# Performance work log

Hardware: AMD Instinct MI355X
Metric: run time of the kernel (lower is better)

## Reference

```python
import jax, jax.numpy as jnp
import numpy as np

B, S, H = 2, 2048, 2048
NH, NKV, HD = 8, 2, 256
WIN = 512
EPS = 1e-6
WAV = 10000.0


def _rms_norm(x, scale=None, eps=EPS):
    # Gemma3n RMSNorm: normalize in float32 over last dim, optional learned scale.
    x32 = x.astype(jnp.float32)
    n = x32 * jax.lax.rsqrt(jnp.mean(x32 * x32, axis=-1, keepdims=True) + eps)
    if scale is not None:
        n = n * scale
    return n.astype(x.dtype)


def _rope(x):
    # keras-hub RotaryEmbedding (half-split rotation). x: [B, S, nheads, hd]
    s, hd = x.shape[1], x.shape[-1]
    inv_freq = 1.0 / (WAV ** (jnp.arange(0, hd, 2, dtype=jnp.float32) / hd))  # [hd/2]
    freqs = jnp.arange(s, dtype=jnp.float32)[:, None] * inv_freq[None, :]      # [S, hd/2]
    cos = jnp.cos(freqs)[None, :, None, :]
    sin = jnp.sin(freqs)[None, :, None, :]
    x1, x2 = jnp.split(x, 2, axis=-1)
    return jnp.concatenate([x1 * cos - x2 * sin, x2 * cos + x1 * sin], axis=-1)


def setup_inputs() -> dict:
    key = jax.random.key(0)
    ks = jax.random.split(key, 8)
    hidden_states = jax.random.normal(ks[0], (B, S, H), dtype=jnp.float32)
    # causal mask [B, S, S]
    causal = jnp.tril(jnp.ones((S, S), dtype=bool))
    attention_mask = jnp.broadcast_to(causal[None], (B, S, S))
    sd = 1.0 / np.sqrt(H)
    Wq = jax.random.normal(ks[1], (H, NH * HD), dtype=jnp.float32) * sd
    Wk = jax.random.normal(ks[2], (H, NKV * HD), dtype=jnp.float32) * sd
    Wv = jax.random.normal(ks[3], (H, NKV * HD), dtype=jnp.float32) * sd
    Wo = jax.random.normal(ks[4], (NH * HD, H), dtype=jnp.float32) * (1.0 / np.sqrt(NH * HD))
    q_scale = jnp.ones((HD,), jnp.float32) + 0.02 * jax.random.normal(ks[5], (HD,), dtype=jnp.float32)
    k_scale = jnp.ones((HD,), jnp.float32) + 0.02 * jax.random.normal(ks[6], (HD,), dtype=jnp.float32)
    return {"hidden_states": hidden_states, "attention_mask": attention_mask,
            "Wq": Wq, "Wk": Wk, "Wv": Wv, "Wo": Wo,
            "q_scale": q_scale, "k_scale": k_scale}


def reference(hidden_states, attention_mask, Wq, Wk, Wv, Wo, q_scale, k_scale):
    b, s, _ = hidden_states.shape
    # Q: proj -> per-head RMSNorm -> RoPE -> [B, NH, S, HD]
    q = (hidden_states @ Wq).reshape(b, s, NH, HD)
    q = jnp.transpose(_rope(_rms_norm(q, q_scale)), (0, 2, 1, 3))
    # K: proj -> RMSNorm -> RoPE; V: proj -> RMSNorm (no scale, no RoPE)
    k = (hidden_states @ Wk).reshape(b, s, NKV, HD)
    k = jnp.transpose(_rope(_rms_norm(k, k_scale)), (0, 2, 1, 3))
    v = jnp.transpose(_rms_norm((hidden_states @ Wv).reshape(b, s, NKV, HD)), (0, 2, 1, 3))
    # GQA repeat_kv (groups = NH // NKV)
    g = NH // NKV
    k = jnp.repeat(k, g, axis=1)
    v = jnp.repeat(v, g, axis=1)
    # scores with scaling = 1.0 (as in source)
    scores = jnp.einsum('bhqd,bhkd->bhqk', q, k)
    # sliding-window band AND user causal mask
    idx = jnp.arange(s)
    band = jnp.abs(idx[:, None] - idx[None, :]) <= (WIN - 1)  # [S, S]
    mask = attention_mask.astype(bool) & band[None]           # [B, S, S]
    scores = jnp.where(mask[:, None], scores, -1e9)
    attn = jax.nn.softmax(scores, axis=-1)
    out = jnp.einsum('bhqk,bhkd->bhqd', attn, v)
    out = jnp.transpose(out, (0, 2, 1, 3)).reshape(b, s, NH * HD)
    return out @ Wo
```

## Files before the change

kernel.cpp:

```cpp
#include <hip/hip_runtime.h>
#include <cstdint>
#include <cstddef>

typedef unsigned short u16;
typedef float floatx4 __attribute__((ext_vector_type(4)));
typedef __bf16 bf16x8 __attribute__((ext_vector_type(8)));

__device__ __forceinline__ u16 f2bf(float f) {
  union { float f; unsigned u; } v;
  v.f = f;
  unsigned u = v.u;
  u += 0x7FFFu + ((u >> 16) & 1u);
  return (u16)(u >> 16);
}
__device__ __forceinline__ float bf2f(u16 h) {
  union { unsigned u; float f; } v;
  v.u = ((unsigned)h) << 16;
  return v.f;
}

#define GLL16(g, l)                                                       \
  __builtin_amdgcn_global_load_lds(                                       \
      (const __attribute__((address_space(1))) void*)(g),                 \
      (__attribute__((address_space(3))) void*)(l), 16, 0, 0)

__global__ __launch_bounds__(256) void prep_all(
    const float* __restrict__ X, u16* __restrict__ Xh, u16* __restrict__ Xl,
    const float* __restrict__ Wq, const float* __restrict__ Wk,
    const float* __restrict__ Wv, const float* __restrict__ Wo,
    u16* __restrict__ Wth, u16* __restrict__ Wot, float* __restrict__ ct,
    float* __restrict__ st) {
  __shared__ u16 T[64][80];
  const int blk = blockIdx.x, t = threadIdx.x;
  if (blk < 4096) {
    const int idx = blk * 256 + t;
    float x[8];
    *(float4*)&x[0] = *(const float4*)(X + (size_t)idx * 8);
    *(float4*)&x[4] = *(const float4*)(X + (size_t)idx * 8 + 4);
    u16 h[8], l[8];
#pragma unroll
    for (int j = 0; j < 8; ++j) {
      h[j] = f2bf(x[j]);
      l[j] = f2bf(x[j] - bf2f(h[j]));
    }
    *(uint4*)(Xh + (size_t)idx * 8) = *(const uint4*)h;
    *(uint4*)(Xl + (size_t)idx * 8) = *(const uint4*)l;
    return;
  }
  if (blk >= 6656) {
    const int idx = (blk - 6656) * 256 + t;
    const int s = idx >> 7, fi = idx & 127;
    const float invf = expf((float)fi * (-9.210340371976184f / 128.f));
    float sv, cv;
    sincosf((float)s * invf, &sv, &cv);
    ct[idx] = cv;
    st[idx] = sv;
    return;
  }
  const float* in;
  u16* out;
  int C, tt, gx, gy;
  if (blk < 5120) {
    in = Wq; out = Wth; C = 2048; tt = blk - 4096; gx = tt & 31; gy = tt >> 5;
  } else if (blk < 5376) {
    in = Wk; out = Wth + (size_t)2048 * 2048; C = 512; tt = blk - 5120;
    gx = tt & 7; gy = tt >> 3;
  } else if (blk < 5632) {
    in = Wv; out = Wth + (size_t)2560 * 2048; C = 512; tt = blk - 5376;
    gx = tt & 7; gy = tt >> 3;
  } else {
    in = Wo; out = Wot; C = 2048; tt = blk - 5632; gx = tt & 31; gy = tt >> 5;
  }
  const int r0 = gy * 64, c0 = gx * 64;
#pragma unroll
  for (int p = 0; p < 4; ++p) {
    const int rl = (t >> 4) + p * 16;
    const int c4 = (t & 15) * 4;
    float4 v = *(const float4*)(in + (size_t)(r0 + rl) * C + c0 + c4);
    T[c4 + 0][rl] = f2bf(v.x);
    T[c4 + 1][rl] = f2bf(v.y);
    T[c4 + 2][rl] = f2bf(v.z);
    T[c4 + 3][rl] = f2bf(v.w);
  }
  __syncthreads();
#pragma unroll
  for (int p = 0; p < 2; ++p) {
    const int cl = (t >> 3) + p * 32;
    const int r8 = (t & 7) * 8;
    *(uint4*)(out + (size_t)(c0 + cl) * 2048 + r0 + r8) =
        *(const uint4*)&T[cl][r8];
  }
}

__global__ __launch_bounds__(256) void gemm_qkv2(
    const u16* __restrict__ Ah, const u16* __restrict__ Al,
    const u16* __restrict__ Bt_all, float* __restrict__ Cq,
    float* __restrict__ Ckv, int K) {
  __shared__ u16 Ash[2][4096], Asl[2][4096], Bs[2][4096];
  const int tid = threadIdx.x;
  const int lane = tid & 63;
  const int wid = tid >> 6;
  const int g = lane >> 4, lc = lane & 15;
  const int gsw = g ^ ((lc >> 1) & 3);
  const int lbs = lc * 32 + gsw * 8;
  const int lin = blockIdx.x;
  const u16* Bt;
  float* C;
  int N, nwg, gridx, lin_s;
  if (lin < 512) {
    Bt = Bt_all; C = Cq; N = 2048; nwg = 512; gridx = 16; lin_s = lin;
  } else {
    Bt = Bt_all + (size_t)2048 * 2048; C = Ckv; N = 1024; nwg = 256;
    gridx = 8; lin_s = lin - 512;
  }
  const int swz = (lin_s & 7) * (nwg >> 3) + (lin_s >> 3);
  const int bm = (swz / gridx) * 128, bn = (swz % gridx) * 128;
  const int wr = (wid >> 1) * 64, wc = (wid & 1) * 64;
  const int xk8 = (((tid & 3) ^ ((tid >> 3) & 3)) * 8);
  const size_t aoff = (size_t)(bm + (tid >> 2)) * K + xk8;
  const size_t boff = (size_t)(bn + (tid >> 2)) * K + xk8;

  floatx4 acc[4][4];
#pragma unroll
  for (int i = 0; i < 4; ++i)
#pragma unroll
    for (int j = 0; j < 4; ++j) acc[i][j] = floatx4{0.f, 0.f, 0.f, 0.f};

  GLL16(Ah + aoff, Ash[0] + tid * 8);
  GLL16(Ah + aoff + (size_t)64 * K, Ash[0] + 2048 + tid * 8);
  GLL16(Al + aoff, Asl[0] + tid * 8);
  GLL16(Al + aoff + (size_t)64 * K, Asl[0] + 2048 + tid * 8);
  GLL16(Bt + boff, Bs[0] + tid * 8);
  GLL16(Bt + boff + (size_t)64 * K, Bs[0] + 2048 + tid * 8);
  int cur = 0;

  for (int k0 = 0; k0 < K; k0 += 32) {
    __syncthreads();
    if (k0 + 32 < K) {
      const int kn = k0 + 32;
      GLL16(Ah + aoff + kn, Ash[cur ^ 1] + tid * 8);
      GLL16(Ah + aoff + (size_t)64 * K + kn, Ash[cur ^ 1] + 2048 + tid * 8);
      GLL16(Al + aoff + kn, Asl[cur ^ 1] + tid * 8);
      GLL16(Al + aoff + (size_t)64 * K + kn, Asl[cur ^ 1] + 2048 + tid * 8);
      GLL16(Bt + boff + kn, Bs[cur ^ 1] + tid * 8);
      GLL16(Bt + boff + (size_t)64 * K + kn, Bs[cur ^ 1] + 2048 + tid * 8);
    }
    bf16x8 afh[4], afl[4], bfr[4];
#pragma unroll
    for (int m = 0; m < 4; ++m) {
      afh[m] = *(const bf16x8*)(Ash[cur] + (wr + m * 16) * 32 + lbs);
      afl[m] = *(const bf16x8*)(Asl[cur] + (wr + m * 16) * 32 + lbs);
    }
#pragma unroll
    for (int n = 0; n < 4; ++n)
      bfr[n] = *(const bf16x8*)(Bs[cur] + (wc + n * 16) * 32 + lbs);
#pragma unroll
    for (int m = 0; m < 4; ++m)
#pragma unroll
      for (int n = 0; n < 4; ++n) {
        acc[m][n] = __builtin_amdgcn_mfma_f32_16x16x32_bf16(afh[m], bfr[n],
                                                            acc[m][n], 0, 0, 0);
        acc[m][n] = __builtin_amdgcn_mfma_f32_16x16x32_bf16(afl[m], bfr[n],
                                                            acc[m][n], 0, 0, 0);
      }
    cur ^= 1;
  }
#pragma unroll
  for (int m = 0; m < 4; ++m)
#pragma unroll
    for (int n = 0; n < 4; ++n) {
      float* Cp = C + (size_t)(bm + wr + m * 16 + g * 4) * N + bn + wc +
                  n * 16 + lc;
#pragma unroll
      for (int r = 0; r < 4; ++r) Cp[(size_t)r * N] = acc[m][n][r];
    }
}

__global__ __launch_bounds__(256) void gemm_bf16(const u16* __restrict__ A,
                                                 const u16* __restrict__ Bt,
                                                 float* __restrict__ C, int M,
                                                 int N, int K) {
  __shared__ u16 As[2][4096];
  __shared__ u16 Bs[2][4096];
  const int tid = threadIdx.x;
  const int lane = tid & 63;
  const int wid = tid >> 6;
  const int g = lane >> 4, lc = lane & 15;
  const int gsw = g ^ ((lc >> 1) & 3);
  const int lbs = lc * 32 + gsw * 8;
  const int nwg = gridDim.x * gridDim.y;
  const int lin = blockIdx.y * gridDim.x + blockIdx.x;
  const int swz = (lin & 7) * (nwg >> 3) + (lin >> 3);
  const int bm = (swz / gridDim.x) * 128, bn = (swz % gridDim.x) * 128;
  const int wr = (wid >> 1) * 64, wc = (wid & 1) * 64;
  const int xk8 = (((tid & 3) ^ ((tid >> 3) & 3)) * 8);
  const u16* Ag = A + (size_t)(bm + (tid >> 2)) * K + xk8;
  const u16* Bg = Bt + (size_t)(bn + (tid >> 2)) * K + xk8;

  floatx4 acc[4][4];
#pragma unroll
  for (int i = 0; i < 4; ++i)
#pragma unroll
    for (int j = 0; j < 4; ++j) acc[i][j] = floatx4{0.f, 0.f, 0.f, 0.f};

  GLL16(Ag, As[0] + tid * 8);
  GLL16(Ag + (size_t)64 * K, As[0] + 2048 + tid * 8);
  GLL16(Bg, Bs[0] + tid * 8);
  GLL16(Bg + (size_t)64 * K, Bs[0] + 2048 + tid * 8);
  int cur = 0;

  for (int k0 = 0; k0 < K; k0 += 32) {
    __syncthreads();
    if (k0 + 32 < K) {
      const int kn = k0 + 32;
      GLL16(Ag + kn, As[cur ^ 1] + tid * 8);
      GLL16(Ag + (size_t)64 * K + kn, As[cur ^ 1] + 2048 + tid * 8);
      GLL16(Bg + kn, Bs[cur ^ 1] + tid * 8);
      GLL16(Bg + (size_t)64 * K + kn, Bs[cur ^ 1] + 2048 + tid * 8);
    }
    bf16x8 af[4], bfr[4];
#pragma unroll
    for (int m = 0; m < 4; ++m)
      af[m] = *(const bf16x8*)(As[cur] + (wr + m * 16) * 32 + lbs);
#pragma unroll
    for (int n = 0; n < 4; ++n)
      bfr[n] = *(const bf16x8*)(Bs[cur] + (wc + n * 16) * 32 + lbs);
#pragma unroll
    for (int m = 0; m < 4; ++m)
#pragma unroll
      for (int n = 0; n < 4; ++n)
        acc[m][n] = __builtin_amdgcn_mfma_f32_16x16x32_bf16(af[m], bfr[n],
                                                            acc[m][n], 0, 0, 0);
    cur ^= 1;
  }
#pragma unroll
  for (int m = 0; m < 4; ++m)
#pragma unroll
    for (int n = 0; n < 4; ++n) {
      float* Cp = C + (size_t)(bm + wr + m * 16 + g * 4) * N + bn + wc +
                  n * 16 + lc;
#pragma unroll
      for (int r = 0; r < 4; ++r) Cp[(size_t)r * N] = acc[m][n][r];
    }
}

__global__ __launch_bounds__(256) void rmsrope2(
    const float* __restrict__ qproj, const float* __restrict__ kvproj,
    u16* __restrict__ qph, u16* __restrict__ qpl, u16* __restrict__ kph,
    u16* __restrict__ kpl, u16* __restrict__ vpk,
    const float* __restrict__ q_scale, const float* __restrict__ k_scale,
    const float* __restrict__ ct, const float* __restrict__ st) {
  __shared__ u16 nh[32][264], nl[32][264];
  const int t = threadIdx.x, lane = t & 63, w = t >> 6;
  const int blk = blockIdx.x;
  const int slot = blk % 12;
  const int rt = blk / 12;
  const int bs0 = rt * 32;
  const int b = bs0 >> 11;
  const int s0 = bs0 & 2047;
  const float* srcb;
  const float* scale = nullptr;
  int srccol, srcstride;
  bool rope;
  if (slot < 8) {
    srcb = qproj; srccol = slot * 256; srcstride = 2048; scale = q_scale;
    rope = true;
  } else if (slot < 10) {
    srcb = kvproj; srccol = (slot - 8) * 256; srcstride = 1024;
    scale = k_scale; rope = true;
  } else {
    srcb = kvproj; srccol = 512 + (slot - 10) * 256; srcstride = 1024;
    rope = false;
  }
  const int d0 = lane * 4;
  float4 sc4 = make_float4(1.f, 1.f, 1.f, 1.f);
  if (scale) sc4 = *(const float4*)(scale + d0);
  const int fi4 = (lane & 31) * 4;

#pragma unroll
  for (int rr = 0; rr < 8; ++rr) {
    const int r = w * 8 + rr;
    const int s = s0 + r;
    float4 x = *(const float4*)(srcb + (size_t)(bs0 + r) * srcstride + srccol +
                                d0);
    float ss = x.x * x.x + x.y * x.y + x.z * x.z + x.w * x.w;
#pragma unroll
    for (int off = 32; off; off >>= 1) ss += __shfl_xor(ss, off);
    const float inv = rsqrtf(ss * (1.f / 256.f) + 1e-6f);
    float4 n;
    n.x = x.x * inv * sc4.x;
    n.y = x.y * inv * sc4.y;
    n.z = x.z * inv * sc4.z;
    n.w = x.w * inv * sc4.w;
    if (rope) {
      float4 p;
      p.x = __shfl_xor(n.x, 32);
      p.y = __shfl_xor(n.y, 32);
      p.z = __shfl_xor(n.z, 32);
      p.w = __shfl_xor(n.w, 32);
      const float4 cv = *(const float4*)(ct + s * 128 + fi4);
      const float4 sv = *(const float4*)(st + s * 128 + fi4);
      if (lane < 32) {
        n.x = n.x * cv.x - p.x * sv.x;
        n.y = n.y * cv.y - p.y * sv.y;
        n.z = n.z * cv.z - p.z * sv.z;
        n.w = n.w * cv.w - p.w * sv.w;
      } else {
        n.x = n.x * cv.x + p.x * sv.x;
        n.y = n.y * cv.y + p.y * sv.y;
        n.z = n.z * cv.z + p.z * sv.z;
        n.w = n.w * cv.w + p.w * sv.w;
      }
    }
    const float nv[4] = {n.x, n.y, n.z, n.w};
#pragma unroll
    for (int j = 0; j < 4; ++j) {
      const u16 hh = f2bf(nv[j]);
      nh[r][d0 + j] = hh;
      nl[r][d0 + j] = f2bf(nv[j] - bf2f(hh));
    }
  }
  __syncthreads();

  if (slot < 8) {
    u16* dh = qph + (((size_t)(b * 8 + slot) * 128 + (s0 >> 4)) * 4096);
    u16* dl = qpl + (((size_t)(b * 8 + slot) * 128 + (s0 >> 4)) * 4096);
#pragma unroll
    for (int p = 0; p < 4; ++p) {
      const int gi = p * 256 + t;
      const int tile = gi >> 9, kc = (gi >> 6) & 7, lc2 = (gi >> 2) & 15,
                gg = gi & 3;
      const int row = tile * 16 + lc2, col = kc * 32 + gg * 8;
      *(uint4*)(dh + (size_t)gi * 8) = *(const uint4*)&nh[row][col];
      *(uint4*)(dl + (size_t)gi * 8) = *(const uint4*)&nl[row][col];
    }
  } else if (slot < 10) {
    const int kvh = slot - 8;
    u16* dh = kph + (((size_t)(b * 2 + kvh) * 64 + (s0 >> 5)) * 8192);
    u16* dl = kpl + (((size_t)(b * 2 + kvh) * 64 + (s0 >> 5)) * 8192);
#pragma unroll
    for (int p = 0; p < 4; ++p) {
      const int gi = p * 256 + t;
      const int kc = gi >> 7, hi = (gi >> 6) & 1, lc2 = (gi >> 2) & 15,
                gg = gi & 3;
      const int ggs = gg ^ ((lc2 >> 1) & 3);
      const int row = hi * 16 + lc2, col = kc * 32 + gg * 8;
      const size_t off = kc * 1024 + hi * 512 + lc2 * 32 + ggs * 8;
      *(uint4*)(dh + off) = *(const uint4*)&nh[row][col];
      *(uint4*)(dl + off) = *(const uint4*)&nl[row][col];
    }
  } else {
    const int kvh = slot - 10;
    u16* dv = vpk + (((size_t)(b * 2 + kvh) * 64 + (s0 >> 5)) * 8192);
#pragma unroll
    for (int p = 0; p < 4; ++p) {
      const int gi = p * 256 + t;
      const int di = gi >> 6, lc2 = (gi >> 2) & 15, gg = gi & 3;
      const int ggs = gg ^ ((lc2 >> 1) & 3);
      u16 tmp[8];
#pragma unroll
      for (int e = 0; e < 8; ++e) tmp[e] = nh[gg * 8 + e][di * 16 + lc2];
      *(uint4*)(dv + (size_t)(di * 512 + lc2 * 32 + ggs * 8)) =
          *(const uint4*)tmp;
    }
  }
}

__global__ __launch_bounds__(512) void attn_mfma5(
    const u16* __restrict__ qph, const u16* __restrict__ qpl,
    const u16* __restrict__ kph, const u16* __restrict__ kpl,
    const u16* __restrict__ vpk, u16* __restrict__ attnb) {
  __shared__ u16 SH[54272];
  u16* const KhB = SH;
  u16* const KlB = SH + 16384;
  u16* const VB = SH + 32768;
  const int tid = threadIdx.x, lane = tid & 63, wid = tid >> 6;
  const int g = lane >> 4, lc = lane & 15;
  const int lbu = lc * 32 + g * 8;
  const int lbs = lc * 32 + (g ^ ((lc >> 1) & 3)) * 8;
  const int lin = blockIdx.x;
  const int swz = (lin & 7) * 32 + (lin >> 3);
  const int qt = swz & 15;
  const int h = (swz >> 4) & 7;
  const int b = swz >> 7;
  const int kvh = h >> 2;
  const int i0b = qt * 128;
  const int i0 = i0b + wid * 16;

  bf16x8 qfh[8], qfl[8];
  {
    const size_t qtb = ((size_t)(b * 8 + h) * 128 + (i0 >> 4)) * 4096 + lbu;
#pragma unroll
    for (int kc = 0; kc < 8; ++kc) {
      qfh[kc] = *(const bf16x8*)(qph + qtb + kc * 512);
      qfl[kc] = *(const bf16x8*)(qpl + qtb + kc * 512);
    }
  }
  floatx4 o[16];
#pragma unroll
  for (int d = 0; d < 16; ++d) o[d] = floatx4{0.f, 0.f, 0.f, 0.f};
  float m_[4] = {-1e20f, -1e20f, -1e20f, -1e20f};
  float l_[4] = {0.f, 0.f, 0.f, 0.f};
  u16* pw = SH + 49152 + wid * 640;

  const int jlo = (i0b >= 512) ? i0b - 512 : 0;
  const int nt = (i0b + 128 - jlo) >> 5;
  const size_t kvbase = (size_t)(b * 2 + kvh) * 64;
  const int t0 = jlo >> 5;

  {
    const size_t tb = (kvbase + t0) * 8192;
    GLL16(kph + tb + tid * 8, KhB + tid * 8);
    GLL16(kph + tb + 4096 + tid * 8, KhB + 4096 + tid * 8);
    GLL16(kpl + tb + tid * 8, KlB + tid * 8);
    GLL16(kpl + tb + 4096 + tid * 8, KlB + 4096 + tid * 8);
    GLL16(vpk + tb + tid * 8, VB + tid * 8);
    GLL16(vpk + tb + 4096 + tid * 8, VB + 4096 + tid * 8);
  }
  int cur = 0;

  for (int t = 0; t < nt; ++t) {
    __syncthreads();
    if (t + 1 < nt) {
      const size_t tb = (kvbase + t0 + t + 1) * 8192;
      const int nb = (cur ^ 1) * 8192;
      GLL16(kph + tb + tid * 8, KhB + nb + tid * 8);
      GLL16(kph + tb + 4096 + tid * 8, KhB + nb + 4096 + tid * 8);
      GLL16(kpl + tb + tid * 8, KlB + nb + tid * 8);
      GLL16(kpl + tb + 4096 + tid * 8, KlB + nb + 4096 + tid * 8);
      GLL16(vpk + tb + tid * 8, VB + nb + tid * 8);
      GLL16(vpk + tb + 4096 + tid * 8, VB + nb + 4096 + tid * 8);
    }
    const int j0 = jlo + t * 32;
    if (!(j0 > i0 + 15 || j0 + 31 < i0 - 511)) {
      const u16* Kh = KhB + cur * 8192;
      const u16* Kl = KlB + cur * 8192;
      floatx4 s0h = floatx4{0.f, 0.f, 0.f, 0.f}, s0x = s0h, s0y = s0h;
      floatx4 s1h = s0h, s1x = s0h, s1y = s0h;
      __builtin_amdgcn_s_setprio(1);
#pragma unroll
      for (int kc = 0; kc < 8; ++kc) {
        const bf16x8 kh0 = *(const bf16x8*)(Kh + kc * 1024 + lbs);
        const bf16x8 kh1 = *(const bf16x8*)(Kh + kc * 1024 + 512 + lbs);
        const bf16x8 kl0 = *(const bf16x8*)(Kl + kc * 1024 + lbs);
        const bf16x8 kl1 = *(const bf16x8*)(Kl + kc * 1024 + 512 + lbs);
        s0h = __builtin_amdgcn_mfma_f32_16x16x32_bf16(qfh[kc], kh0, s0h, 0, 0, 0);
        s1h = __builtin_amdgcn_mfma_f32_16x16x32_bf16(qfh[kc], kh1, s1h, 0, 0, 0);
        s0x = __builtin_amdgcn_mfma_f32_16x16x32_bf16(qfh[kc], kl0, s0x, 0, 0, 0);
        s1x = __builtin_amdgcn_mfma_f32_16x16x32_bf16(qfh[kc], kl1, s1x, 0, 0, 0);
        s0y = __builtin_amdgcn_mfma_f32_16x16x32_bf16(qfl[kc], kh0, s0y, 0, 0, 0);
        s1y = __builtin_amdgcn_mfma_f32_16x16x32_bf16(qfl[kc], kh1, s1y, 0, 0, 0);
      }
      __builtin_amdgcn_s_setprio(0);
      floatx4 s0 = s0h + s0x + s0y;
      floatx4 s1 = s1h + s1x + s1y;
      if (!(j0 + 31 <= i0 && (i0 + 15) - j0 <= 511)) {
        const int ja = j0 + lc, jb_ = j0 + 16 + lc;
#pragma unroll
        for (int r = 0; r < 4; ++r) {
          const int i = i0 + g * 4 + r;
          if (ja > i || i - ja > 511) s0[r] = -1e30f;
          if (jb_ > i || i - jb_ > 511) s1[r] = -1e30f;
        }
      }
      float rmax[4], p0[4], p1[4], sc[4], rs[4];
#pragma unroll
      for (int r = 0; r < 4; ++r) rmax[r] = fmaxf(s0[r], s1[r]);
#pragma unroll
      for (int off = 1; off < 16; off <<= 1)
#pragma unroll
        for (int r = 0; r < 4; ++r)
          rmax[r] = fmaxf(rmax[r], __shfl_xor(rmax[r], off));
#pragma unroll
      for (int r = 0; r < 4; ++r) {
        const float mn = fmaxf(m_[r], rmax[r]);
        sc[r] = __expf(m_[r] - mn);
        m_[r] = mn;
        p0[r] = __expf(s0[r] - mn);
        p1[r] = __expf(s1[r] - mn);
        rs[r] = p0[r] + p1[r];
      }
#pragma unroll
      for (int off = 1; off < 16; off <<= 1)
#pragma unroll
        for (int r = 0; r < 4; ++r) rs[r] += __shfl_xor(rs[r], off);
#pragma unroll
      for (int r = 0; r < 4; ++r) l_[r] = l_[r] * sc[r] + rs[r];
#pragma unroll
      for (int r = 0; r < 4; ++r) {
        pw[(g * 4 + r) * 40 + lc] = f2bf(p0[r]);
        pw[(g * 4 + r) * 40 + 16 + lc] = f2bf(p1[r]);
      }
#pragma unroll
      for (int d = 0; d < 16; ++d)
#pragma unroll
        for (int r = 0; r < 4; ++r) o[d][r] *= sc[r];
      const bf16x8 pf = *(const bf16x8*)(pw + lc * 40 + g * 8);
      const u16* Vt = VB + cur * 8192;
      __builtin_amdgcn_s_setprio(1);
#pragma unroll
      for (int d = 0; d < 16; ++d)
        o[d] = __builtin_amdgcn_mfma_f32_16x16x32_bf16(
            pf, *(const bf16x8*)(Vt + d * 512 + lbs), o[d], 0, 0, 0);
      __builtin_amdgcn_s_setprio(0);
    }
    cur ^= 1;
  }
  float rinv[4];
#pragma unroll
  for (int r = 0; r < 4; ++r) rinv[r] = 1.f / l_[r];
  __syncthreads();
  u16* ow = SH + wid * 4224;
#pragma unroll
  for (int d = 0; d < 16; ++d)
#pragma unroll
    for (int r = 0; r < 4; ++r)
      ow[(g * 4 + r) * 264 + d * 16 + lc] = f2bf(o[d][r] * rinv[r]);
  u16* orow = attnb + ((size_t)(b * 2048 + i0) * 2048 + h * 256);
#pragma unroll
  for (int p = 0; p < 8; ++p) {
    const int gi = p * 64 + lane;
    const int row = gi >> 5, ch = gi & 31;
    *(uint4*)(orow + (size_t)row * 2048 + ch * 8) =
        *(const uint4*)(ow + row * 264 + ch * 8);
  }
}

extern "C" void kernel_launch(void* const* d_in, const int* in_sizes, int n_in,
                              void* d_out, int out_size, void* d_ws,
                              size_t ws_size, hipStream_t stream) {
  (void)in_sizes;
  (void)n_in;
  (void)out_size;
  (void)ws_size;
  const float* X = (const float*)d_in[0];
  const float* Wq = (const float*)d_in[2];
  const float* Wk = (const float*)d_in[3];
  const float* Wv = (const float*)d_in[4];
  const float* Wo = (const float*)d_in[5];
  const float* qs = (const float*)d_in[6];
  const float* ks = (const float*)d_in[7];
  float* out = (float*)d_out;
  char* ws = (char*)d_ws;

  float* kvproj = (float*)(ws);
  u16* attnb = (u16*)(ws);
  u16* Xh = (u16*)(ws + 16777216);
  u16* qph = Xh;
  u16* Xl = (u16*)(ws + 33554432);
  u16* qpl = Xl;
  u16* Wth = (u16*)(ws + 50331648);
  u16* kph = (u16*)(ws + 50331648);
  u16* kpl = (u16*)(ws + 54525952);
  u16* vpk = (u16*)(ws + 58720256);
  float* ct = (float*)(ws + 62914560);
  float* st = (float*)(ws + 63963136);
  u16* Wot = (u16*)(ws + 75497472);
  float* qproj = out;

  prep_all<<<7680, 256, 0, stream>>>(X, Xh, Xl, Wq, Wk, Wv, Wo, Wth, Wot, ct,
                                     st);
  gemm_qkv2<<<768, 256, 0, stream>>>(Xh, Xl, Wth, qproj, kvproj, 2048);
  rmsrope2<<<12 * 128, 256, 0, stream>>>(qproj, kvproj, qph, qpl, kph, kpl,
                                         vpk, qs, ks, ct, st);
  attn_mfma5<<<256, 512, 0, stream>>>(qph, qpl, kph, kpl, vpk, attnb);
  gemm_bf16<<<dim3(16, 32), 256, 0, stream>>>(attnb, Wot, out, 4096, 2048,
                                              2048);
}
```

Baseline: 259.7 us.

## Load V fragments directly to registers and add lazy softmax rescaling

```diff
diff --git a/kernel.cpp b/kernel.cpp
--- a/kernel.cpp
+++ b/kernel.cpp
@@ -366,14 +366,13 @@
   }
 }
 
-__global__ __launch_bounds__(512) void attn_mfma5(
+__global__ __launch_bounds__(512) void attn_mfma6(
     const u16* __restrict__ qph, const u16* __restrict__ qpl,
     const u16* __restrict__ kph, const u16* __restrict__ kpl,
     const u16* __restrict__ vpk, u16* __restrict__ attnb) {
-  __shared__ u16 SH[54272];
+  __shared__ u16 SH[37888];
   u16* const KhB = SH;
   u16* const KlB = SH + 16384;
-  u16* const VB = SH + 32768;
   const int tid = threadIdx.x, lane = tid & 63, wid = tid >> 6;
   const int g = lane >> 4, lc = lane & 15;
   const int lbu = lc * 32 + g * 8;
@@ -401,7 +400,7 @@
   for (int d = 0; d < 16; ++d) o[d] = floatx4{0.f, 0.f, 0.f, 0.f};
   float m_[4] = {-1e20f, -1e20f, -1e20f, -1e20f};
   float l_[4] = {0.f, 0.f, 0.f, 0.f};
-  u16* pw = SH + 49152 + wid * 640;
+  u16* pw = SH + 32768 + wid * 640;
 
   const int jlo = (i0b >= 512) ? i0b - 512 : 0;
   const int nt = (i0b + 128 - jlo) >> 5;
@@ -414,13 +413,20 @@
     GLL16(kph + tb + 4096 + tid * 8, KhB + 4096 + tid * 8);
     GLL16(kpl + tb + tid * 8, KlB + tid * 8);
     GLL16(kpl + tb + 4096 + tid * 8, KlB + 4096 + tid * 8);
-    GLL16(vpk + tb + tid * 8, VB + tid * 8);
-    GLL16(vpk + tb + 4096 + tid * 8, VB + 4096 + tid * 8);
   }
   int cur = 0;
 
   for (int t = 0; t < nt; ++t) {
     __syncthreads();
+    const int j0 = jlo + t * 32;
+    const bool live = !(j0 > i0 + 15 || j0 + 31 < i0 - 511);
+    bf16x8 vf[16];
+    if (live) {
+      const u16* vg = vpk + (kvbase + t0 + t) * 8192;
+#pragma unroll
+      for (int d = 0; d < 16; ++d)
+        vf[d] = *(const bf16x8*)(vg + d * 512 + lbs);
+    }
     if (t + 1 < nt) {
       const size_t tb = (kvbase + t0 + t + 1) * 8192;
       const int nb = (cur ^ 1) * 8192;
@@ -428,11 +434,8 @@
       GLL16(kph + tb + 4096 + tid * 8, KhB + nb + 4096 + tid * 8);
       GLL16(kpl + tb + tid * 8, KlB + nb + tid * 8);
       GLL16(kpl + tb + 4096 + tid * 8, KlB + nb + 4096 + tid * 8);
-      GLL16(vpk + tb + tid * 8, VB + nb + tid * 8);
-      GLL16(vpk + tb + 4096 + tid * 8, VB + nb + 4096 + tid * 8);
-    }
-    const int j0 = jlo + t * 32;
-    if (!(j0 > i0 + 15 || j0 + 31 < i0 - 511)) {
+    }
+    if (live) {
       const u16* Kh = KhB + cur * 8192;
       const u16* Kl = KlB + cur * 8192;
       floatx4 s0h = floatx4{0.f, 0.f, 0.f, 0.f}, s0x = s0h, s0y = s0h;
@@ -463,7 +466,7 @@
           if (jb_ > i || i - jb_ > 511) s1[r] = -1e30f;
         }
       }
-      float rmax[4], p0[4], p1[4], sc[4], rs[4];
+      float rmax[4], p0[4], p1[4], rs[4];
 #pragma unroll
       for (int r = 0; r < 4; ++r) rmax[r] = fmaxf(s0[r], s1[r]);
 #pragma unroll
@@ -471,37 +474,55 @@
 #pragma unroll
         for (int r = 0; r < 4; ++r)
           rmax[r] = fmaxf(rmax[r], __shfl_xor(rmax[r], off));
-#pragma unroll
-      for (int r = 0; r < 4; ++r) {
-        const float mn = fmaxf(m_[r], rmax[r]);
-        sc[r] = __expf(m_[r] - mn);
-        m_[r] = mn;
-        p0[r] = __expf(s0[r] - mn);
-        p1[r] = __expf(s1[r] - mn);
-        rs[r] = p0[r] + p1[r];
+      float dm = rmax[0] - m_[0];
+#pragma unroll
+      for (int r = 1; r < 4; ++r) dm = fmaxf(dm, rmax[r] - m_[r]);
+      if (__all(dm <= 8.f)) {
+#pragma unroll
+        for (int r = 0; r < 4; ++r) {
+          p0[r] = __expf(s0[r] - m_[r]);
+          p1[r] = __expf(s1[r] - m_[r]);
+          rs[r] = p0[r] + p1[r];
+        }
+#pragma unroll
+        for (int off = 1; off < 16; off <<= 1)
+#pragma unroll
+          for (int r = 0; r < 4; ++r) rs[r] += __shfl_xor(rs[r], off);
+#pragma unroll
+        for (int r = 0; r < 4; ++r) l_[r] += rs[r];
+      } else {
+        float sc[4];
+#pragma unroll
+        for (int r = 0; r < 4; ++r) {
+          const float mn = fmaxf(m_[r], rmax[r]);
+          sc[r] = __expf(m_[r] - mn);
+          m_[r] = mn;
+          p0[r] = __expf(s0[r] - mn);
+          p1[r] = __expf(s1[r] - mn);
+          rs[r] = p0[r] + p1[r];
+        }
+#pragma unroll
+        for (int off = 1; off < 16; off <<= 1)
+#pragma unroll
+          for (int r = 0; r < 4; ++r) rs[r] += __shfl_xor(rs[r], off);
+#pragma unroll
+        for (int r = 0; r < 4; ++r) l_[r] = l_[r] * sc[r] + rs[r];
+#pragma unroll
+        for (int d = 0; d < 16; ++d)
+#pragma unroll
+          for (int r = 0; r < 4; ++r) o[d][r] *= sc[r];
       }
-#pragma unroll
-      for (int off = 1; off < 16; off <<= 1)
-#pragma unroll
-        for (int r = 0; r < 4; ++r) rs[r] += __shfl_xor(rs[r], off);
-#pragma unroll
-      for (int r = 0; r < 4; ++r) l_[r] = l_[r] * sc[r] + rs[r];
 #pragma unroll
       for (int r = 0; r < 4; ++r) {
         pw[(g * 4 + r) * 40 + lc] = f2bf(p0[r]);
         pw[(g * 4 + r) * 40 + 16 + lc] = f2bf(p1[r]);
       }
+      const bf16x8 pf = *(const bf16x8*)(pw + lc * 40 + g * 8);
+      __builtin_amdgcn_s_setprio(1);
 #pragma unroll
       for (int d = 0; d < 16; ++d)
-#pragma unroll
-        for (int r = 0; r < 4; ++r) o[d][r] *= sc[r];
-      const bf16x8 pf = *(const bf16x8*)(pw + lc * 40 + g * 8);
-      const u16* Vt = VB + cur * 8192;
-      __builtin_amdgcn_s_setprio(1);
-#pragma unroll
-      for (int d = 0; d < 16; ++d)
-        o[d] = __builtin_amdgcn_mfma_f32_16x16x32_bf16(
-            pf, *(const bf16x8*)(Vt + d * 512 + lbs), o[d], 0, 0, 0);
+        o[d] = __builtin_amdgcn_mfma_f32_16x16x32_bf16(pf, vf[d], o[d], 0, 0,
+                                                       0);
       __builtin_amdgcn_s_setprio(0);
     }
     cur ^= 1;
@@ -563,7 +584,7 @@
   gemm_qkv2<<<768, 256, 0, stream>>>(Xh, Xl, Wth, qproj, kvproj, 2048);
   rmsrope2<<<12 * 128, 256, 0, stream>>>(qproj, kvproj, qph, qpl, kph, kpl,
                                          vpk, qs, ks, ct, st);
-  attn_mfma5<<<256, 512, 0, stream>>>(qph, qpl, kph, kpl, vpk, attnb);
+  attn_mfma6<<<256, 512, 0, stream>>>(qph, qpl, kph, kpl, vpk, attnb);
   gemm_bf16<<<dim3(16, 32), 256, 0, stream>>>(attnb, Wot, out, 4096, 2048,
                                               2048);
 }
```

Result: slower. 450.9 us (+73.6%).
